# Optimization experiments

Measured on AMD Instinct MI355X. Metric: run time of the kernel, lower is better.

## Reference

```python
import jax, jax.numpy as jnp
from jax import lax
import numpy as np

EPS = 1e-5
DN = ('NCHW', 'OIHW', 'NCHW')


def conv_s2(x, w):
    # Conv2d k=4 s=2 p=1, no bias
    return lax.conv_general_dilated(x, w, (2, 2), [(1, 1), (1, 1)], dimension_numbers=DN)


def deconv_s2(x, w):
    # ConvTranspose2d k=4 s=2 p=1; torch weight layout (in, out, kH, kW)
    w_ = jnp.flip(w, (2, 3)).transpose(1, 0, 2, 3)  # -> (out, in, kH, kW)
    return lax.conv_general_dilated(x, w_, (1, 1), [(2, 2), (2, 2)],
                                    lhs_dilation=(2, 2), dimension_numbers=DN)


def bn_train(x, gamma, beta):
    # BatchNorm2d in training mode: batch stats over (N, H, W), biased variance
    m = jnp.mean(x, axis=(0, 2, 3), keepdims=True)
    v = jnp.var(x, axis=(0, 2, 3), keepdims=True)
    g = gamma.reshape(1, -1, 1, 1)
    b = beta.reshape(1, -1, 1, 1)
    return (x - m) * jax.lax.rsqrt(v + EPS) * g + b


def lrelu(x):
    return jnp.where(x >= 0, x, 0.2 * x)


def setup_inputs() -> dict:
    key = jax.random.key(0)
    ks = jax.random.split(key, 32)
    nef = 64
    d = {}
    d['x'] = jax.random.normal(ks[0], (256, 3, 64, 64), dtype=jnp.float32)
    # encoder conv weights (O, I, 4, 4), init N(0, 0.02)
    d['w1'] = 0.02 * jax.random.normal(ks[1], (nef, 3, 4, 4), jnp.float32)
    d['w2'] = 0.02 * jax.random.normal(ks[2], (nef * 2, nef, 4, 4), jnp.float32)
    d['w3'] = 0.02 * jax.random.normal(ks[3], (nef * 4, nef * 2, 4, 4), jnp.float32)
    d['w4'] = 0.02 * jax.random.normal(ks[4], (nef * 8, nef * 4, 4, 4), jnp.float32)
    # bn params: weight ~ N(1, 0.02), bias = 0
    for i, c in enumerate([nef, nef * 2, nef * 4, nef * 8]):
        d[f'g{i+1}'] = 1.0 + 0.02 * jax.random.normal(ks[5 + i], (c,), jnp.float32)
        d[f'b{i+1}'] = jnp.zeros((c,), jnp.float32)
    # 512 channel-wise Linear(16,16): torch default init U(-1/4, 1/4)
    bound = 1.0 / 4.0
    d['cw_w'] = jax.random.uniform(ks[9], (512, 16, 16), jnp.float32, -bound, bound)
    d['cw_b'] = jax.random.uniform(ks[10], (512, 16), jnp.float32, -bound, bound)
    # decoder deconv weights in torch layout (in, out, 4, 4)
    d['dw1'] = 0.02 * jax.random.normal(ks[11], (nef * 8, nef * 4, 4, 4), jnp.float32)
    d['dw2'] = 0.02 * jax.random.normal(ks[12], (nef * 4, nef * 2, 4, 4), jnp.float32)
    d['dw3'] = 0.02 * jax.random.normal(ks[13], (nef * 2, nef, 4, 4), jnp.float32)
    d['dw4'] = 0.02 * jax.random.normal(ks[14], (nef, 3, 4, 4), jnp.float32)
    for i, c in enumerate([nef * 4, nef * 2, nef]):
        d[f'dg{i+1}'] = 1.0 + 0.02 * jax.random.normal(ks[15 + i], (c,), jnp.float32)
        d[f'db{i+1}'] = jnp.zeros((c,), jnp.float32)
    return d


def reference(x, w1, w2, w3, w4, g1, b1, g2, b2, g3, b3, g4, b4,
              cw_w, cw_b, dw1, dw2, dw3, dw4, dg1, db1, dg2, db2, dg3, db3):
    h = lrelu(bn_train(conv_s2(x, w1), g1, b1))
    h = lrelu(bn_train(conv_s2(h, w2), g2, b2))
    h = lrelu(bn_train(conv_s2(h, w3), g3, b3))
    h = lrelu(bn_train(conv_s2(h, w4), g4, b4))  # (B, 512, 4, 4)
    B, C, H, W = h.shape
    flat = h.reshape(B, C, H * W)  # (B, 512, 16)
    # per-channel Linear: y[b,c,t] = sum_s flat[b,c,s] * cw_w[c,t,s] + cw_b[c,t]
    flat = jnp.einsum('bcs,cts->bct', flat, cw_w) + cw_b[None, :, :]
    h = flat.reshape(B, C, H, W)
    h = jax.nn.relu(bn_train(deconv_s2(h, dw1), dg1, db1))
    h = jax.nn.relu(bn_train(deconv_s2(h, dw2), dg2, db2))
    h = jax.nn.relu(bn_train(deconv_s2(h, dw3), dg3, db3))
    return jnp.tanh(deconv_s2(h, dw4))
```

## Files before the change

### kernel.cpp

```cpp
#include <hip/hip_runtime.h>
#include <math.h>

typedef _Float16 f16;
typedef __attribute__((ext_vector_type(8))) _Float16 f16x8;
typedef __attribute__((ext_vector_type(16))) float f32x16;

union U64x2 { unsigned long long u[2]; f16x8 v; };
union Q16   { uint4 q; unsigned long long u[2]; };

constexpr int ilog2c(int x) { return x <= 1 ? 0 : 1 + ilog2c(x >> 1); }

__device__ __forceinline__ float fast_tanh(float x) {
    float e = __expf(2.f * x);
    return (e - 1.f) / (e + 1.f);
}

__device__ __forceinline__ void barrier_no_vmdrain() {
    asm volatile("s_waitcnt lgkmcnt(0)" ::: "memory");
    __builtin_amdgcn_sched_barrier(0);
    __builtin_amdgcn_s_barrier();
    __builtin_amdgcn_sched_barrier(0);
}

template<int CIN,int IH,int IW,int OH,int OW,int COUT,int COB,int SPT,int KS,
         int CO_FR,bool DEC,bool PAIR>
__global__ __launch_bounds__(256,2) void mfma_conv(
    const f16* __restrict__ xin, const f16* __restrict__ wp,
    f16* __restrict__ out16, float* __restrict__ out32, size_t ps,
    float* __restrict__ psumF, float* __restrict__ psqF)
{
    constexpr int OHo  = DEC ? OH/2 : OH;
    constexpr int OWo  = DEC ? OW/2 : OW;
    constexpr int KTOT = CIN * (DEC ? 4 : 16);
    constexpr int CH   = (KTOT/64) / KS;
    constexpr int RPT  = CIN / 64;
    constexpr int RSH  = (RPT==1?0:RPT==2?1:RPT==4?2:3);
    constexpr int WSTR = CIN * 16;
    constexpr int TPR  = 256 / COB;
    constexpr int SPB  = OHo * OWo;
    constexpr int LSPB = ilog2c(SPB);
    constexpr int LOWo = ilog2c(OWo);

    static_assert(!PAIR || (RPT >= 2 && CH % 2 == 0), "PAIR needs RPT>=2");
    constexpr int CHU  = PAIR ? CH/2 : CH;
    constexpr int RW   = PAIR ? 32 : 16;
    constexpr int PM   = PAIR ? 15 : 7;
    constexpr int KKN  = PAIR ? 8 : 4;
    constexpr int XU4  = PAIR ? 16 : 8;
    constexpr int WSEG = (PAIR ? 128 : 64)/TPR;
    constexpr int WU4  = WSEG / 8;

    __shared__ unsigned long long Xs[SPT*RW];
    __shared__ unsigned long long Wls[COB*RW];

    const int t   = threadIdx.x;
    const int bx  = blockIdx.x;
    const int cob = blockIdx.y;
    const int bz  = blockIdx.z;
    const int par = DEC ? (bz & 3) : 0;
    const int ks  = DEC ? (bz >> 2) : bz;
    const int poh = par >> 1, pw = par & 1;

    const int gsp_s = bx*SPT + t;
    const int img_s = gsp_s >> LSPB;
    const int r_s   = gsp_s & (SPB-1);
    const int oy_s  = r_s >> LOWo;
    const int ox_s  = r_s & (OWo-1);

    const int wco   = t / TPR;
    const int wpart = t % TPR;
    const f16* wbase = wp + (size_t)(cob*COB + wco)*WSTR + wpart*WSEG;

    const int wave = t >> 6, lane = t & 63, half = lane >> 5, l31 = lane & 31;
    const int co_w = (wave >> 1) * (CO_FR*32);
    const int sp_w = (wave & 1) * 128;
    const int swz  = l31 & PM;

    f32x16 acc[CO_FR][4];
    #pragma unroll
    for (int i = 0; i < CO_FR; ++i)
        #pragma unroll
        for (int b = 0; b < 4; ++b)
            #pragma unroll
            for (int r = 0; r < 16; ++r) acc[i][b][r] = 0.f;

    uint4 xreg[XU4];
    uint4 wreg[WU4];

    auto issue = [&](int cc) {
        const int gc  = ks*CH + (PAIR ? 2*cc : cc);
        const int tap = gc >> RSH;
        const int ci0 = (gc & (RPT-1)) << 6;
        int kh, kw, ih, iw;
        if (DEC) {
            const int t2h = tap >> 1, t2w = tap & 1;
            kh = (1-poh) + 2*t2h; kw = (1-pw) + 2*t2w;
            ih = oy_s + poh - t2h; iw = ox_s + pw - t2w;
        } else {
            kh = tap >> 2; kw = tap & 3;
            ih = 2*oy_s - 1 + kh; iw = 2*ox_s - 1 + kw;
        }
        const int woff = (kh*4 + kw)*CIN + ci0;
        const uint4* wsrc = (const uint4*)(wbase + woff);
        #pragma unroll
        for (int j = 0; j < WU4; ++j) wreg[j] = wsrc[j];
        const bool ok = (unsigned)ih < (unsigned)IH && (unsigned)iw < (unsigned)IW;
        if (ok) {
            const uint4* xsrc = (const uint4*)
                (xin + ((size_t)(img_s*IH + ih)*IW + iw)*CIN + ci0);
            #pragma unroll
            for (int j = 0; j < XU4; ++j) xreg[j] = xsrc[j];
        } else {
            #pragma unroll
            for (int j = 0; j < XU4; ++j) xreg[j] = uint4{0u,0u,0u,0u};
        }
    };

    issue(0);

    for (int cc = 0; cc < CHU; ++cc) {
        if (cc) barrier_no_vmdrain();

        #pragma unroll
        for (int j = 0; j < WU4; ++j) {
            Q16 v; v.q = wreg[j];
            const int lp = wpart*WU4 + j;
            const int u0 = wco*RW + ((lp ^ (wco & PM)) << 1);
            Wls[u0]   = v.u[0];
            Wls[u0+1] = v.u[1];
        }
        {
            #pragma unroll
            for (int j = 0; j < XU4; ++j) {
                Q16 v; v.q = xreg[j];
                const int u0 = t*RW + ((j ^ (t & PM)) << 1);
                Xs[u0]   = v.u[0];
                Xs[u0+1] = v.u[1];
            }
        }

        if (cc + 1 < CHU) issue(cc + 1);

        asm volatile("s_waitcnt lgkmcnt(0)" ::: "memory");
        __builtin_amdgcn_sched_barrier(0);
        __builtin_amdgcn_s_barrier();
        __builtin_amdgcn_sched_barrier(0);

        #pragma unroll
        for (int kk = 0; kk < KKN; ++kk) {
            const int so = ((kk*2 + half) ^ swz) << 1;
            f16x8 wf[CO_FR], xf[4];
            #pragma unroll
            for (int i = 0; i < CO_FR; ++i) {
                U64x2 u; const int rw = (co_w + i*32 + l31)*RW + so;
                u.u[0] = Wls[rw]; u.u[1] = Wls[rw+1]; wf[i] = u.v;
            }
            #pragma unroll
            for (int b = 0; b < 4; ++b) {
                U64x2 u; const int rx = (sp_w + b*32 + l31)*RW + so;
                u.u[0] = Xs[rx]; u.u[1] = Xs[rx+1]; xf[b] = u.v;
            }
            #pragma unroll
            for (int i = 0; i < CO_FR; ++i)
                #pragma unroll
                for (int b = 0; b < 4; ++b)
                    acc[i][b] = __builtin_amdgcn_mfma_f32_32x32x16_f16(
                        xf[b], wf[i], acc[i][b], 0, 0, 0);
        }
    }

    #pragma unroll
    for (int b = 0; b < 4; ++b) {
        #pragma unroll
        for (int q = 0; q < 4; ++q) {
            #pragma unroll
            for (int r2 = 0; r2 < 4; ++r2) {
                const int sp_loc = sp_w + b*32 + q*8 + 4*half + r2;
                const int gsp    = bx*SPT + sp_loc;
                size_t base;
                if (DEC) {
                    const int img = gsp >> LSPB;
                    const int r   = gsp & (SPB-1);
                    const int oh  = 2*(r >> LOWo) + poh;
                    const int ow  = 2*(r & (OWo-1)) + pw;
                    base = ((size_t)(img*OH + oh)*OW + ow)*COUT + cob*COB;
                } else {
                    base = (size_t)gsp*COUT + cob*COB;
                }
                #pragma unroll
                for (int i = 0; i < CO_FR; ++i) {
                    const int co_l = co_w + i*32 + l31;
                    const float v  = acc[i][b][q*4 + r2];
                    if (KS == 1) out16[base + co_l] = (_Float16)v;
                    else         out32[(size_t)ks*ps + base + co_l] = v;
                }
            }
        }
    }

    if (KS == 1 && psumF != nullptr) {
        float sArr[CO_FR], qArr[CO_FR];
        #pragma unroll
        for (int i = 0; i < CO_FR; ++i) {
            float s = 0.f, q = 0.f;
            #pragma unroll
            for (int b = 0; b < 4; ++b)
                #pragma unroll
                for (int r = 0; r < 16; ++r) {
                    const float v = acc[i][b][r];
                    s += v; q += v * v;
                }
            s += __shfl_down(s, 32);
            q += __shfl_down(q, 32);
            sArr[i] = s; qArr[i] = q;
        }
        __syncthreads();
        float* LS = (float*)Xs;
        float* LQ = LS + 4*CO_FR*32;
        if (half == 0) {
            #pragma unroll
            for (int i = 0; i < CO_FR; ++i) {
                LS[(wave*CO_FR + i)*32 + l31] = sArr[i];
                LQ[(wave*CO_FR + i)*32 + l31] = qArr[i];
            }
        }
        __syncthreads();
        if (t < COB) {
            constexpr int KSH = (CO_FR == 1 ? 5 : 6);
            const int k  = t >> KSH;
            const int ii = (CO_FR == 1) ? 0 : ((t >> 5) & 1);
            const int l  = t & 31;
            const int i0 = ((2*k)  *CO_FR + ii)*32 + l;
            const int i1 = ((2*k+1)*CO_FR + ii)*32 + l;
            atomicAdd(psumF + cob*COB + t, LS[i0] + LS[i1]);
            atomicAdd(psqF  + cob*COB + t, LQ[i0] + LQ[i1]);
        }
    }
}

__global__ __launch_bounds__(256,2) void conv1_mfma(
    const f16* __restrict__ xp, const f16* __restrict__ wp,
    f16* __restrict__ out, float* __restrict__ psumF, float* __restrict__ psqF)
{
    __shared__ unsigned long long Xs[256*16];
    __shared__ unsigned long long Wls[64*16];
    const int t = threadIdx.x, bx = blockIdx.x;

    {
        const int r = t >> 2, part = t & 3;
        const uint4* src = (const uint4*)(wp + r*64 + part*16);
        Q16 v0; v0.q = src[0];
        Q16 v1; v1.q = src[1];
        const int a0 = r*16 + (((part*2)   ^ (r & 7)) << 1);
        const int a1 = r*16 + (((part*2+1) ^ (r & 7)) << 1);
        Wls[a0]   = v0.u[0]; Wls[a0+1] = v0.u[1];
        Wls[a1]   = v1.u[0]; Wls[a1+1] = v1.u[1];
    }
    {
        const int gsp = bx*256 + t;
        const int n = gsp >> 10, r = gsp & 1023;
        const int oy = r >> 5, ox = r & 31;
        const int ih0 = 2*oy - 1, iw0 = 2*ox - 1;
        #pragma unroll
        for (int tap = 0; tap < 16; ++tap) {
            const int ih = ih0 + (tap >> 2), iw = iw0 + (tap & 3);
            unsigned long long v = 0ull;
            if ((unsigned)ih < 64u && (unsigned)iw < 64u)
                v = *(const unsigned long long*)(xp + (((size_t)n*64 + ih)*64 + iw)*4);
            const int u = t*16 + (((tap >> 1) ^ (t & 7)) << 1) + (tap & 1);
            Xs[u] = v;
        }
    }
    __syncthreads();

    const int wave = t >> 6, lane = t & 63, half = lane >> 5, l31 = lane & 31;
    const int co_w = (wave >> 1) * 32;
    const int sp_w = (wave & 1) * 128;
    const int swz  = l31 & 7;

    f32x16 acc[4];
    #pragma unroll
    for (int b = 0; b < 4; ++b)
        #pragma unroll
        for (int r = 0; r < 16; ++r) acc[b][r] = 0.f;

    #pragma unroll
    for (int kk = 0; kk < 4; ++kk) {
        const int so = ((kk*2 + half) ^ swz) << 1;
        U64x2 uw; const int rw = (co_w + l31)*16 + so;
        uw.u[0] = Wls[rw]; uw.u[1] = Wls[rw+1];
        #pragma unroll
        for (int b = 0; b < 4; ++b) {
            U64x2 ux; const int rx = (sp_w + b*32 + l31)*16 + so;
            ux.u[0] = Xs[rx]; ux.u[1] = Xs[rx+1];
            acc[b] = __builtin_amdgcn_mfma_f32_32x32x16_f16(
                ux.v, uw.v, acc[b], 0, 0, 0);
        }
    }
    #pragma unroll
    for (int b = 0; b < 4; ++b)
        #pragma unroll
        for (int q = 0; q < 4; ++q)
            #pragma unroll
            for (int r2 = 0; r2 < 4; ++r2) {
                const int sp_loc = sp_w + b*32 + q*8 + 4*half + r2;
                out[(size_t)(bx*256 + sp_loc)*64 + co_w + l31] =
                    (_Float16)acc[b][q*4 + r2];
            }

    float s = 0.f, q = 0.f;
    #pragma unroll
    for (int b = 0; b < 4; ++b)
        #pragma unroll
        for (int r = 0; r < 16; ++r) {
            const float v = acc[b][r];
            s += v; q += v * v;
        }
    s += __shfl_down(s, 32);
    q += __shfl_down(q, 32);
    __syncthreads();
    {
        float* LS = (float*)Xs;
        float* LQ = LS + 128;
        if (half == 0) {
            LS[wave*32 + l31] = s;
            LQ[wave*32 + l31] = q;
        }
        __syncthreads();
        if (t < 64) {
            const int k = t >> 5, l = t & 31;
            atomicAdd(psumF + t, LS[(2*k)*32 + l] + LS[(2*k+1)*32 + l]);
            atomicAdd(psqF  + t, LQ[(2*k)*32 + l] + LQ[(2*k+1)*32 + l]);
        }
    }
}

__global__ __launch_bounds__(256,2) void deconv4_mfma(
    const f16* __restrict__ xin, const f16* __restrict__ wp,
    float* __restrict__ out)
{
    __shared__ unsigned long long Xs[256*16];
    __shared__ unsigned long long Wls[32*16];

    const int t   = threadIdx.x;
    const int bx  = blockIdx.x;
    const int par = blockIdx.y;
    const int poh = par >> 1, pw = par & 1;

    const int gsp_s = bx*256 + t;
    const int img_s = gsp_s >> 10;
    const int r_s   = gsp_s & 1023;
    const int oy_s  = r_s >> 5;
    const int ox_s  = r_s & 31;

    const int wco   = t >> 3;
    const int wpart = t & 7;

    const int wave = t >> 6, lane = t & 63, half = lane >> 5, l31 = lane & 31;
    const int sp_w = wave * 64;
    const int swz  = l31 & 7;

    f32x16 acc[2];
    #pragma unroll
    for (int b = 0; b < 2; ++b)
        #pragma unroll
        for (int r = 0; r < 16; ++r) acc[b][r] = 0.f;

    uint4 xreg[8];
    uint4 wreg1;

    auto issue4 = [&](int cc) {
        const int t2h = cc >> 1, t2w = cc & 1;
        const int kh = (1-poh) + 2*t2h, kw = (1-pw) + 2*t2w;
        const int ih = oy_s + poh - t2h, iw = ox_s + pw - t2w;
        wreg1 = *(const uint4*)(wp + wco*1024 + (kh*4 + kw)*64 + wpart*8);
        const bool ok = (unsigned)ih < 32u && (unsigned)iw < 32u;
        if (ok) {
            const uint4* src = (const uint4*)
                (xin + ((size_t)(img_s*32 + ih)*32 + iw)*64);
            #pragma unroll
            for (int j = 0; j < 8; ++j) xreg[j] = src[j];
        } else {
            #pragma unroll
            for (int j = 0; j < 8; ++j) xreg[j] = uint4{0u,0u,0u,0u};
        }
    };

    issue4(0);

    for (int cc = 0; cc < 4; ++cc) {
        if (cc) barrier_no_vmdrain();
        {
            Q16 v; v.q = wreg1;
            const int u0 = wco*16 + ((wpart ^ (wco & 7)) << 1);
            Wls[u0] = v.u[0]; Wls[u0+1] = v.u[1];
        }
        {
            #pragma unroll
            for (int j = 0; j < 8; ++j) {
                Q16 v; v.q = xreg[j];
                const int u0 = t*16 + ((j ^ (t & 7)) << 1);
                Xs[u0]   = v.u[0];
                Xs[u0+1] = v.u[1];
            }
        }
        if (cc + 1 < 4) issue4(cc + 1);
        asm volatile("s_waitcnt lgkmcnt(0)" ::: "memory");
        __builtin_amdgcn_sched_barrier(0);
        __builtin_amdgcn_s_barrier();
        __builtin_amdgcn_sched_barrier(0);

        #pragma unroll
        for (int kk = 0; kk < 4; ++kk) {
            const int so = ((kk*2 + half) ^ swz) << 1;
            U64x2 uw; const int rw = l31*16 + so;
            uw.u[0] = Wls[rw]; uw.u[1] = Wls[rw+1];
            #pragma unroll
            for (int b = 0; b < 2; ++b) {
                U64x2 ux; const int rx = (sp_w + b*32 + l31)*16 + so;
                ux.u[0] = Xs[rx]; ux.u[1] = Xs[rx+1];
                acc[b] = __builtin_amdgcn_mfma_f32_32x32x16_f16(
                    uw.v, ux.v, acc[b], 0, 0, 0);
            }
        }
    }

    if (half == 0) {
        #pragma unroll
        for (int b = 0; b < 2; ++b) {
            const int gsp = bx*256 + sp_w + b*32 + l31;
            const int img = gsp >> 10;
            const int r   = gsp & 1023;
            const int oh  = 2*(r >> 5) + poh;
            const int ow  = 2*(r & 31) + pw;
            #pragma unroll
            for (int co = 0; co < 3; ++co)
                out[(((size_t)img*3 + co)*64 + oh)*64 + ow] =
                    fast_tanh(acc[b][co]);
        }
    }
}

__global__ __launch_bounds__(256) void prep_x(
    const float* __restrict__ x, f16* __restrict__ xp)
{
    const int i = blockIdx.x*256 + threadIdx.x;
    const int n = i >> 12, p = i & 4095;
    const float* b = x + (size_t)n*12288 + p;
    union { _Float16 h[4]; unsigned long long u; } o;
    o.h[0] = (_Float16)b[0];
    o.h[1] = (_Float16)b[4096];
    o.h[2] = (_Float16)b[8192];
    o.h[3] = (_Float16)0.f;
    *(unsigned long long*)(xp + (size_t)i*4) = o.u;
}

__global__ __launch_bounds__(256) void prep_w1(
    const float* __restrict__ w1, f16* __restrict__ wp)
{
    const int e = blockIdx.x*256 + threadIdx.x;
    const int co = e >> 6, k = e & 63, tap = k >> 2, ci = k & 3;
    const float v = (ci < 3) ? w1[(co*3 + ci)*16 + tap] : 0.f;
    wp[e] = (_Float16)v;
}

__global__ __launch_bounds__(256) void prep_w4(
    const float* __restrict__ dw4, f16* __restrict__ wp)
{
    const int e = blockIdx.x*256 + threadIdx.x;
    const int co = e >> 10, r = e & 1023, khw = r >> 6, ci = r & 63;
    const float v = (co < 3) ? dw4[(ci*3 + co)*16 + khw] : 0.f;
    wp[e] = (_Float16)v;
}

__global__ __launch_bounds__(256) void prep_w(
    const float* __restrict__ w2, const float* __restrict__ w3,
    const float* __restrict__ w4, const float* __restrict__ dw1,
    const float* __restrict__ dw2, const float* __restrict__ dw3,
    f16* __restrict__ dst)
{
    const int e = blockIdx.x*256 + threadIdx.x;
    float v;
    if (e < 131072) {
        int co = e >> 10, r = e & 1023, khw = r >> 6, ci = r & 63;
        v = w2[(co*64 + ci)*16 + khw];
    } else if (e < 655360) {
        int l = e - 131072;
        int co = l >> 11, r = l & 2047, khw = r >> 7, ci = r & 127;
        v = w3[(co*128 + ci)*16 + khw];
    } else if (e < 2752512) {
        int l = e - 655360;
        int co = l >> 12, r = l & 4095, khw = r >> 8, ci = r & 255;
        v = w4[(co*256 + ci)*16 + khw];
    } else if (e < 4849664) {
        int l = e - 2752512;
        int co = l >> 13, r = l & 8191, khw = r >> 9, ci = r & 511;
        v = dw1[(ci*256 + co)*16 + khw];
    } else if (e < 5373952) {
        int l = e - 4849664;
        int co = l >> 12, r = l & 4095, khw = r >> 8, ci = r & 255;
        v = dw2[(ci*128 + co)*16 + khw];
    } else {
        int l = e - 5373952;
        int co = l >> 11, r = l & 2047, khw = r >> 7, ci = r & 127;
        v = dw3[(ci*64 + co)*16 + khw];
    }
    dst[e] = (_Float16)v;
}

template<typename T, int P>
__global__ __launch_bounds__(256) void bn_partial(
    const T* __restrict__ x, size_t ps, float* __restrict__ psum,
    float* __restrict__ psq, int C, int rowsPerS, int S)
{
    const int s = blockIdx.x;
    const int c = (blockIdx.y << 6) + (threadIdx.x & 63);
    float a = 0.f, q = 0.f;
    const int rEnd = (s + 1) * rowsPerS;
    for (int r = s*rowsPerS + (threadIdx.x >> 6); r < rEnd; r += 4) {
        float v = 0.f;
        #pragma unroll
        for (int p = 0; p < P; ++p)
            v += (float)x[p*ps + (size_t)r * C + c];
        a += v; q += v * v;
    }
    __shared__ float ls[256], lq[256];
    ls[threadIdx.x] = a; lq[threadIdx.x] = q;
    __syncthreads();
    if (threadIdx.x < 64) {
        a = ls[threadIdx.x] + ls[threadIdx.x+64] + ls[threadIdx.x+128] + ls[threadIdx.x+192];
        q = lq[threadIdx.x] + lq[threadIdx.x+64] + lq[threadIdx.x+128] + lq[threadIdx.x+192];
        psum[c * S + s] = a; psq[c * S + s] = q;
    }
}

__global__ __launch_bounds__(256) void bn_finalize(
    const float* __restrict__ psum, const float* __restrict__ psq,
    const float* __restrict__ gamma, const float* __restrict__ beta,
    float* __restrict__ scale, float* __restrict__ shift,
    int C, int S, float inv_count)
{
    int c = blockIdx.x * 256 + threadIdx.x;
    if (c >= C) return;
    float s = 0.f, q = 0.f;
    for (int i = 0; i < S; ++i) { s += psum[c*S + i]; q += psq[c*S + i]; }
    float m   = s * inv_count;
    float var = q * inv_count - m * m;
    var = var < 0.f ? 0.f : var;
    float sc = gamma[c] * rsqrtf(var + 1e-5f);
    scale[c] = sc;
    shift[c] = beta[c] - m * sc;
}

__global__ __launch_bounds__(256) void bn_act16f(
    f16* __restrict__ x, const float* __restrict__ psum, const float* __restrict__ psq,
    const float* __restrict__ gamma, const float* __restrict__ beta,
    int Cmask, float inv_count, float slope, size_t n8)
{
    const size_t base = (size_t)blockIdx.x*256 + threadIdx.x;
    const int c0 = (int)((base * 8) & (size_t)Cmask);
    float sc[8], sh[8];
    #pragma unroll
    for (int j = 0; j < 8; ++j) {
        const int c = c0 + j;
        float m   = psum[c] * inv_count;
        float var = psq[c] * inv_count - m * m;
        var = var < 0.f ? 0.f : var;
        float s = gamma[c] * rsqrtf(var + 1e-5f);
        sc[j] = s;
        sh[j] = beta[c] - m * s;
    }
    const size_t stride = (size_t)gridDim.x * 256;
    for (size_t i = base; i < n8; i += stride) {
        union { uint4 u; _Float16 h[8]; } a;
        a.u = *(const uint4*)(x + i*8);
        #pragma unroll
        for (int j = 0; j < 8; ++j) {
            float v = (float)a.h[j] * sc[j] + sh[j];
            a.h[j] = (_Float16)(v >= 0.f ? v : slope * v);
        }
        *(uint4*)(x + i*8) = a.u;
    }
}

template<int P>
__global__ __launch_bounds__(256) void bn_act32(
    const float* __restrict__ x, size_t ps, f16* __restrict__ y,
    const float* __restrict__ sc, const float* __restrict__ sh,
    int Cmask, float slope)
{
    const size_t i8 = ((size_t)blockIdx.x*256 + threadIdx.x) * 8;
    float xv[8] = {0,0,0,0,0,0,0,0};
    #pragma unroll
    for (int p = 0; p < P; ++p) {
        float4 v0 = *(const float4*)(x + p*ps + i8);
        float4 v1 = *(const float4*)(x + p*ps + i8 + 4);
        xv[0]+=v0.x; xv[1]+=v0.y; xv[2]+=v0.z; xv[3]+=v0.w;
        xv[4]+=v1.x; xv[5]+=v1.y; xv[6]+=v1.z; xv[7]+=v1.w;
    }
    union { uint4 u; _Float16 h[8]; } a;
    const int c0 = (int)(i8 & (size_t)Cmask);
    #pragma unroll
    for (int j = 0; j < 8; ++j) {
        float v = xv[j] * sc[c0+j] + sh[c0+j];
        a.h[j] = (_Float16)(v >= 0.f ? v : slope * v);
    }
    *(uint4*)(y + i8) = a.u;
}

__global__ __launch_bounds__(256) void chanlin16(
    const f16* __restrict__ in, const float* __restrict__ w,
    const float* __restrict__ bias, f16* __restrict__ out)
{
    const int i = blockIdx.x*256 + threadIdx.x;
    const int c  = i & 511;
    const int bt = i >> 9;
    const int b  = bt >> 4, tt = bt & 15;
    const f16* src = in + ((size_t)b*16)*512 + c;
    const float* wr = w + ((size_t)c*16 + tt)*16;
    float acc = bias[c*16 + tt];
    #pragma unroll
    for (int s = 0; s < 16; ++s)
        acc = fmaf((float)src[s*512], wr[s], acc);
    out[i] = (_Float16)acc;
}

extern "C" void kernel_launch(void* const* d_in, const int* in_sizes, int n_in,
                              void* d_out, int out_size, void* d_ws, size_t ws_size,
                              hipStream_t stream)
{
    const float* x   = (const float*)d_in[0];
    const float* w1  = (const float*)d_in[1];
    const float* w2  = (const float*)d_in[2];
    const float* w3  = (const float*)d_in[3];
    const float* w4  = (const float*)d_in[4];
    const float* g1  = (const float*)d_in[5];
    const float* b1  = (const float*)d_in[6];
    const float* g2  = (const float*)d_in[7];
    const float* b2  = (const float*)d_in[8];
    const float* g3  = (const float*)d_in[9];
    const float* b3  = (const float*)d_in[10];
    const float* g4  = (const float*)d_in[11];
    const float* b4  = (const float*)d_in[12];
    const float* cww = (const float*)d_in[13];
    const float* cwb = (const float*)d_in[14];
    const float* dw1 = (const float*)d_in[15];
    const float* dw2 = (const float*)d_in[16];
    const float* dw3 = (const float*)d_in[17];
    const float* dw4 = (const float*)d_in[18];
    const float* dg1 = (const float*)d_in[19];
    const float* db1 = (const float*)d_in[20];
    const float* dg2 = (const float*)d_in[21];
    const float* db2 = (const float*)d_in[22];
    const float* dg3 = (const float*)d_in[23];
    const float* db3 = (const float*)d_in[24];

    char* WS = (char*)d_ws;
    float* psum  = (float*)WS;
    float* psq   = (float*)(WS + 65536);
    float* scale = (float*)(WS + 131072);
    float* shift = (float*)(WS + 133120);
    float* fst   = (float*)(WS + 196608);
    f16* slotA   = (f16*)(WS + 262144);
    f16* slotB   = (f16*)(WS + 262144 + 33554432);
    f16* wprep   = (f16*)(WS + 84148224);
    f16* wprep1  = wprep + 5505024;
    f16* wprep4  = wprep1 + 4096;

    f16*   A_hi  = slotA + 8388608;
    float* pB    = (float*)slotB;
    f16*   xpack = slotA;

    float* fs0 = fst;          float* fs1 = fst + 1024;
    float* fs2 = fst + 2048;   float* fs4 = fst + 4096;
    float* fs5 = fst + 5120;   float* fs6 = fst + 6144;

    hipMemsetAsync(fst, 0, 28672, stream);
    prep_w<<<21504, 256, 0, stream>>>(w2, w3, w4, dw1, dw2, dw3, wprep);
    prep_w1<<<16, 256, 0, stream>>>(w1, wprep1);
    prep_w4<<<128, 256, 0, stream>>>(dw4, wprep4);
    prep_x<<<4096, 256, 0, stream>>>(x, xpack);

    conv1_mfma<<<1024, 256, 0, stream>>>(xpack, wprep1, slotB, fs0, fs0 + 512);
    bn_act16f<<<2048, 256, 0, stream>>>(slotB, fs0, fs0 + 512, g1, b1, 63,
                                        1.f/262144.f, 0.2f, (size_t)2097152);

    mfma_conv<64,32,32,16,16,128, 128,256,1,2,false,false><<<dim3(256,1,1), 256, 0, stream>>>(
        slotB, wprep, slotA, nullptr, 0, fs1, fs1 + 512);
    bn_act16f<<<2048, 256, 0, stream>>>(slotA, fs1, fs1 + 512, g2, b2, 127,
                                        1.f/65536.f, 0.2f, (size_t)1048576);

    mfma_conv<128,16,16,8,8,256, 64,256,1,1,false,false><<<dim3(64,4,1), 256, 0, stream>>>(
        slotA, wprep + 131072, A_hi, nullptr, 0, fs2, fs2 + 512);
    bn_act16f<<<2048, 256, 0, stream>>>(A_hi, fs2, fs2 + 512, g3, b3, 255,
                                        1.f/16384.f, 0.2f, (size_t)524288);

    mfma_conv<256,8,8,4,4,512, 128,256,4,2,false,false><<<dim3(16,4,4), 256, 0, stream>>>(
        A_hi, wprep + 655360, nullptr, pB, (size_t)2097152, nullptr, nullptr);
    bn_partial<float,4><<<dim3(32,8), 256, 0, stream>>>(pB, (size_t)2097152, psum, psq, 512, 128, 32);
    bn_finalize<<<2, 256, 0, stream>>>(psum, psq, g4, b4, scale, shift, 512, 32, 1.f/4096.f);
    bn_act32<4><<<1024, 256, 0, stream>>>(pB, (size_t)2097152, slotA, scale, shift, 511, 0.2f);

    chanlin16<<<8192, 256, 0, stream>>>(slotA, cww, cwb, slotB);

    mfma_conv<512,4,4,8,8,256, 64,256,1,1,true,false><<<dim3(16,4,4), 256, 0, stream>>>(
        slotB, wprep + 2752512, A_hi, nullptr, 0, fs4, fs4 + 512);
    bn_act16f<<<2048, 256, 0, stream>>>(A_hi, fs4, fs4 + 512, dg1, db1, 255,
                                        1.f/16384.f, 0.f, (size_t)524288);

    mfma_conv<256,8,8,16,16,128, 128,256,1,2,true,false><<<dim3(64,1,4), 256, 0, stream>>>(
        A_hi, wprep + 4849664, slotB, nullptr, 0, fs5, fs5 + 512);
    bn_act16f<<<2048, 256, 0, stream>>>(slotB, fs5, fs5 + 512, dg2, db2, 127,
                                        1.f/65536.f, 0.f, (size_t)1048576);

    mfma_conv<128,16,16,32,32,64, 64,256,1,1,true,true><<<dim3(256,1,4), 256, 0, stream>>>(
        slotB, wprep + 5373952, slotA, nullptr, 0, fs6, fs6 + 512);
    bn_act16f<<<2048, 256, 0, stream>>>(slotA, fs6, fs6 + 512, dg3, db3, 63,
                                        1.f/262144.f, 0.f, (size_t)2097152);

    deconv4_mfma<<<dim3(1024,4), 256, 0, stream>>>(slotA, wprep4, (float*)d_out);
}
```

Measured before the change: 550.9 us.

## Merge four deconv output parities into one block sharing input tiles

```diff
diff --git a/kernel.cpp b/kernel.cpp
--- a/kernel.cpp
+++ b/kernel.cpp
@@ -340,12 +340,10 @@
     float* __restrict__ out)
 {
     __shared__ unsigned long long Xs[256*16];
-    __shared__ unsigned long long Wls[32*16];
+    __shared__ unsigned long long Wls[4][32*16];
 
     const int t   = threadIdx.x;
     const int bx  = blockIdx.x;
-    const int par = blockIdx.y;
-    const int poh = par >> 1, pw = par & 1;
 
     const int gsp_s = bx*256 + t;
     const int img_s = gsp_s >> 10;
@@ -360,20 +358,19 @@
     const int sp_w = wave * 64;
     const int swz  = l31 & 7;
 
-    f32x16 acc[2];
-    #pragma unroll
-    for (int b = 0; b < 2; ++b)
-        #pragma unroll
-        for (int r = 0; r < 16; ++r) acc[b][r] = 0.f;
+    f32x16 acc[4][2];
+    #pragma unroll
+    for (int p = 0; p < 4; ++p)
+        #pragma unroll
+        for (int b = 0; b < 2; ++b)
+            #pragma unroll
+            for (int r = 0; r < 16; ++r) acc[p][b][r] = 0.f;
 
     uint4 xreg[8];
-    uint4 wreg1;
-
-    auto issue4 = [&](int cc) {
-        const int t2h = cc >> 1, t2w = cc & 1;
-        const int kh = (1-poh) + 2*t2h, kw = (1-pw) + 2*t2w;
-        const int ih = oy_s + poh - t2h, iw = ox_s + pw - t2w;
-        wreg1 = *(const uint4*)(wp + wco*1024 + (kh*4 + kw)*64 + wpart*8);
+
+    auto issueX = [&](int oid) {
+        const int dh = oid/3 - 1, dw = oid%3 - 1;
+        const int ih = oy_s + dh, iw = ox_s + dw;
         const bool ok = (unsigned)ih < 32u && (unsigned)iw < 32u;
         if (ok) {
             const uint4* src = (const uint4*)
@@ -386,57 +383,102 @@
         }
     };
 
-    issue4(0);
-
-    for (int cc = 0; cc < 4; ++cc) {
-        if (cc) barrier_no_vmdrain();
-        {
-            Q16 v; v.q = wreg1;
-            const int u0 = wco*16 + ((wpart ^ (wco & 7)) << 1);
-            Wls[u0] = v.u[0]; Wls[u0+1] = v.u[1];
-        }
-        {
-            #pragma unroll
-            for (int j = 0; j < 8; ++j) {
-                Q16 v; v.q = xreg[j];
-                const int u0 = t*16 + ((j ^ (t & 7)) << 1);
-                Xs[u0]   = v.u[0];
-                Xs[u0+1] = v.u[1];
-            }
-        }
-        if (cc + 1 < 4) issue4(cc + 1);
+    issueX(0);
+
+    #pragma unroll
+    for (int oid = 0; oid < 9; ++oid) {
+        const int dh = oid/3 - 1, dw = oid%3 - 1;
+        const int nH = (dh == 0) ? 2 : 1;
+        const int nW = (dw == 0) ? 2 : 1;
+
+        if (oid) barrier_no_vmdrain();
+
+        uint4 wregc[4];
+        #pragma unroll
+        for (int ch = 0; ch < 2; ++ch) {
+            #pragma unroll
+            for (int cw = 0; cw < 2; ++cw) {
+                if (ch < nH && cw < nW) {
+                    const int poh_ = (dh == -1) ? 0 : (dh == 1) ? 1 : ch;
+                    const int pw_  = (dw == -1) ? 0 : (dw == 1) ? 1 : cw;
+                    const int kh   = (1 - poh_) + 2*(poh_ - dh);
+                    const int kw   = (1 - pw_)  + 2*(pw_  - dw);
+                    wregc[ch*2+cw] = *(const uint4*)
+                        (wp + wco*1024 + (kh*4 + kw)*64 + wpart*8);
+                }
+            }
+        }
+
+        #pragma unroll
+        for (int j = 0; j < 8; ++j) {
+            Q16 v; v.q = xreg[j];
+            const int u0 = t*16 + ((j ^ (t & 7)) << 1);
+            Xs[u0]   = v.u[0];
+            Xs[u0+1] = v.u[1];
+        }
+        #pragma unroll
+        for (int ch = 0; ch < 2; ++ch) {
+            #pragma unroll
+            for (int cw = 0; cw < 2; ++cw) {
+                if (ch < nH && cw < nW) {
+                    Q16 v; v.q = wregc[ch*2+cw];
+                    const int u0 = wco*16 + ((wpart ^ (wco & 7)) << 1);
+                    Wls[ch*2+cw][u0]   = v.u[0];
+                    Wls[ch*2+cw][u0+1] = v.u[1];
+                }
+            }
+        }
+
+        if (oid + 1 < 9) issueX(oid + 1);
+
         asm volatile("s_waitcnt lgkmcnt(0)" ::: "memory");
         __builtin_amdgcn_sched_barrier(0);
         __builtin_amdgcn_s_barrier();
         __builtin_amdgcn_sched_barrier(0);
 
         #pragma unroll
-        for (int kk = 0; kk < 4; ++kk) {
-            const int so = ((kk*2 + half) ^ swz) << 1;
-            U64x2 uw; const int rw = l31*16 + so;
-            uw.u[0] = Wls[rw]; uw.u[1] = Wls[rw+1];
+        for (int ch = 0; ch < 2; ++ch) {
+            #pragma unroll
+            for (int cw = 0; cw < 2; ++cw) {
+                if (ch < nH && cw < nW) {
+                    const int poh_ = (dh == -1) ? 0 : (dh == 1) ? 1 : ch;
+                    const int pw_  = (dw == -1) ? 0 : (dw == 1) ? 1 : cw;
+                    const int p    = poh_*2 + pw_;
+                    #pragma unroll
+                    for (int kk = 0; kk < 4; ++kk) {
+                        const int so = ((kk*2 + half) ^ swz) << 1;
+                        U64x2 uw; const int rw = l31*16 + so;
+                        uw.u[0] = Wls[ch*2+cw][rw];
+                        uw.u[1] = Wls[ch*2+cw][rw+1];
+                        #pragma unroll
+                        for (int b = 0; b < 2; ++b) {
+                            U64x2 ux; const int rx = (sp_w + b*32 + l31)*16 + so;
+                            ux.u[0] = Xs[rx]; ux.u[1] = Xs[rx+1];
+                            acc[p][b] = __builtin_amdgcn_mfma_f32_32x32x16_f16(
+                                uw.v, ux.v, acc[p][b], 0, 0, 0);
+                        }
+                    }
+                }
+            }
+        }
+    }
+
+    if (half == 0) {
+        #pragma unroll
+        for (int p = 0; p < 4; ++p) {
+            const int poh = p >> 1, pw = p & 1;
             #pragma unroll
             for (int b = 0; b < 2; ++b) {
-                U64x2 ux; const int rx = (sp_w + b*32 + l31)*16 + so;
-                ux.u[0] = Xs[rx]; ux.u[1] = Xs[rx+1];
-                acc[b] = __builtin_amdgcn_mfma_f32_32x32x16_f16(
-                    uw.v, ux.v, acc[b], 0, 0, 0);
-            }
-        }
-    }
-
-    if (half == 0) {
-        #pragma unroll
-        for (int b = 0; b < 2; ++b) {
-            const int gsp = bx*256 + sp_w + b*32 + l31;
-            const int img = gsp >> 10;
-            const int r   = gsp & 1023;
-            const int oh  = 2*(r >> 5) + poh;
-            const int ow  = 2*(r & 31) + pw;
-            #pragma unroll
-            for (int co = 0; co < 3; ++co)
-                out[(((size_t)img*3 + co)*64 + oh)*64 + ow] =
-                    fast_tanh(acc[b][co]);
+                const int gsp = bx*256 + sp_w + b*32 + l31;
+                const int img = gsp >> 10;
+                const int r   = gsp & 1023;
+                const int oh  = 2*(r >> 5) + poh;
+                const int ow  = 2*(r & 31) + pw;
+                #pragma unroll
+                for (int co = 0; co < 3; ++co)
+                    out[(((size_t)img*3 + co)*64 + oh)*64 + ow] =
+                        fast_tanh(acc[p][b][co]);
+            }
         }
     }
 }
@@ -718,5 +760,5 @@
     bn_act16f<<<2048, 256, 0, stream>>>(slotA, fs6, fs6 + 512, dg3, db3, 63,
                                         1.f/262144.f, 0.f, (size_t)2097152);
 
-    deconv4_mfma<<<dim3(1024,4), 256, 0, stream>>>(slotA, wprep4, (float*)d_out);
-}
+    deconv4_mfma<<<1024, 256, 0, stream>>>(slotA, wprep4, (float*)d_out);
+}
```

Measured after the change: 535.5 us. -2.8%, faster.
